# Optimization experiments

Measured on AMD Instinct MI355X. Metric: run time of the kernel, lower is better.

The kernel has to match this reference:

```python
import jax, jax.numpy as jnp
import numpy as np

DIM = 96
HEADS = 6
HEAD_DIM = DIM // HEADS
WIN = 8
N = WIN * WIN           # tokens per window
B_ = 4096               # num_windows * batch
TABLE = (2 * WIN - 1) ** 2  # 225


def setup_inputs() -> dict:
    key = jax.random.key(0)
    ks = jax.random.split(key, 7)
    x = jax.random.normal(ks[0], (B_, N, DIM), dtype=jnp.float32)
    rpi = jax.random.randint(ks[1], (N, N), 0, TABLE)
    qkv_w = jax.random.normal(ks[2], (3 * DIM, DIM), dtype=jnp.float32) * 0.02
    qkv_b = jnp.zeros((3 * DIM,), dtype=jnp.float32)
    proj_w = jax.random.normal(ks[3], (DIM, DIM), dtype=jnp.float32) * 0.02
    proj_b = jnp.zeros((DIM,), dtype=jnp.float32)
    rpb_table = jax.random.normal(ks[4], (TABLE, HEADS), dtype=jnp.float32) * 0.02
    return {"x": x, "rpi": rpi, "qkv_w": qkv_w, "qkv_b": qkv_b,
            "proj_w": proj_w, "proj_b": proj_b, "rpb_table": rpb_table}


def reference(x, rpi, qkv_w, qkv_b, proj_w, proj_b, rpb_table):
    b_, n, c = x.shape
    scale = HEAD_DIM ** -0.5
    # qkv projection: (b_, n, 3, H, hd)
    qkv = (x @ qkv_w.T + qkv_b).reshape(b_, n, 3, HEADS, HEAD_DIM)
    qkv = jnp.transpose(qkv, (2, 0, 3, 1, 4))  # (3, b_, H, n, hd)
    q, k, v = qkv[0], qkv[1], qkv[2]
    attn = jnp.einsum('bhnd,bhmd->bhnm', q * scale, k)
    # relative position bias gather: (n, n, H) -> (H, n, n)
    bias = jnp.transpose(rpb_table[rpi], (2, 0, 1))
    attn = jax.nn.softmax(attn + bias[None], axis=-1)
    out = jnp.einsum('bhnm,bhmd->bnhd', attn, v).reshape(b_, n, c)
    return out @ proj_w.T + proj_b
```

## Files before the change

### kernel.cpp

```cpp
#include <hip/hip_runtime.h>

#define NWIN 4096
#define DIM 96
#define HEADS 6
#define NTOK 64

typedef __bf16 bf16x8 __attribute__((ext_vector_type(8)));
typedef __bf16 bf16x4 __attribute__((ext_vector_type(4)));
typedef short  s16x4  __attribute__((ext_vector_type(4)));
typedef float  f32x4  __attribute__((ext_vector_type(4)));

#define WS_QKVW 0
#define WS_PROJW 55296
#define WS_BIAS 73728
#define WS_TOTAL 172032

__device__ __forceinline__ f32x4 mfma32(bf16x8 a, bf16x8 b, f32x4 c) {
  return __builtin_amdgcn_mfma_f32_16x16x32_bf16(a, b, c, 0, 0, 0);
}
__device__ __forceinline__ f32x4 mfma16k(bf16x4 a, bf16x4 b, f32x4 c) {
  return __builtin_amdgcn_mfma_f32_16x16x16bf16_1k(
      __builtin_bit_cast(s16x4, a), __builtin_bit_cast(s16x4, b), c, 0, 0, 0);
}

__device__ __forceinline__ bf16x8 cvt8(const float* p) {
  const float4* q = (const float4*)p;
  float4 a = q[0];
  float4 b = q[1];
  bf16x8 r;
  r[0] = (__bf16)a.x; r[1] = (__bf16)a.y; r[2] = (__bf16)a.z; r[3] = (__bf16)a.w;
  r[4] = (__bf16)b.x; r[5] = (__bf16)b.y; r[6] = (__bf16)b.z; r[7] = (__bf16)b.w;
  return r;
}

__global__ void prep_kernel(const float* __restrict__ qkv_w,
                            const float* __restrict__ proj_w,
                            const float* __restrict__ rpb,
                            const int* __restrict__ rpi,
                            char* __restrict__ ws) {
  int i = blockIdx.x * blockDim.x + threadIdx.x;
  __bf16* qw = (__bf16*)(ws + WS_QKVW);
  __bf16* pw = (__bf16*)(ws + WS_PROJW);
  float* bias = (float*)(ws + WS_BIAS);
  if (i < 288 * 96) qw[i] = (__bf16)qkv_w[i];
  int j = i - 288 * 96;
  if (j >= 0 && j < 96 * 96) pw[j] = (__bf16)proj_w[j];
  int t = i - (288 * 96 + 96 * 96);
  if (t >= 0 && t < HEADS * 16 * 64 * 4) {
    int r = t & 3;
    int lane = (t >> 2) & 63;
    int ba = (t >> 8) & 15;
    int h = t >> 12;
    int bq = ba >> 2, a = ba & 3;
    int l16 = lane & 15, lq = lane >> 4;
    int qrow = 16 * bq + l16;
    int kcol = 16 * a + 4 * lq + r;
    bias[t] = rpb[rpi[qrow * 64 + kcol] * HEADS + h];
  }
}

template <bool USE_WS>
__global__ __launch_bounds__(384, 4) void win_attn(
    const float* __restrict__ x,
    const int* __restrict__ rpi,
    const float* __restrict__ qkv_w,
    const float* __restrict__ qkv_b,
    const float* __restrict__ proj_w,
    const float* __restrict__ proj_b,
    const float* __restrict__ rpb,
    const char* __restrict__ ws,
    float* __restrict__ out) {
  __shared__ __align__(16) __bf16 lds[6656 + HEADS * 1152];

  const int tid = (int)threadIdx.x;
  const int wv = tid >> 6;
  const int lane = tid & 63;
  const int l16 = lane & 15;
  const int lq = lane >> 4;
  const int b = (int)blockIdx.x;

  __bf16* xfrag = lds;
  __bf16* ao = lds;
  __bf16* vh = lds + 6656 + wv * 1152;
  __bf16* Pt = vh;

  const float* xw = x + (size_t)b * (NTOK * DIM);
  const __bf16* qwb = (const __bf16*)(ws + WS_QKVW);
  const __bf16* pwb = (const __bf16*)(ws + WS_PROJW);
  const float4* bias4 = (const float4*)(ws + WS_BIAS) + (wv << 10);

#pragma unroll
  for (int ff = 0; ff < 2; ++ff) {
    const int f = 2 * wv + ff;
    const int mt = f / 3, ks = f - 3 * mt;
    bf16x8 v = cvt8(xw + (16 * mt + l16) * DIM + 32 * ks + 8 * lq);
    *(bf16x8*)(xfrag + (f * 64 + lane) * 8) = v;
  }
  __syncthreads();

#define XV(mt, ks) (*(const bf16x8*)(xfrag + (((mt) * 3 + (ks)) * 64 + lane) * 8))

  bf16x4 kb[4];
  {
    const int frow = (HEADS + wv) * 16;
    bf16x8 wb[3];
#pragma unroll
    for (int ks = 0; ks < 3; ++ks) {
      if constexpr (USE_WS)
        wb[ks] = *(const bf16x8*)(qwb + (frow + l16) * 96 + 32 * ks + 8 * lq);
      else
        wb[ks] = cvt8(qkv_w + (frow + l16) * 96 + 32 * ks + 8 * lq);
    }
    const float4 kb4 = *(const float4*)(qkv_b + frow + 4 * lq);
    const float kbv[4] = {kb4.x, kb4.y, kb4.z, kb4.w};
#pragma unroll
    for (int mt = 0; mt < 4; ++mt) {
      f32x4 acc = {0.f, 0.f, 0.f, 0.f};
#pragma unroll
      for (int ks = 0; ks < 3; ++ks) acc = mfma32(wb[ks], XV(mt, ks), acc);
#pragma unroll
      for (int r = 0; r < 4; ++r) kb[mt][r] = (__bf16)(acc[r] + kbv[r]);
    }
  }

  bf16x4 qv4[4];
  {
    const int frow = wv * 16;
    bf16x8 wb[3];
#pragma unroll
    for (int ks = 0; ks < 3; ++ks) {
      if constexpr (USE_WS)
        wb[ks] = *(const bf16x8*)(qwb + (frow + l16) * 96 + 32 * ks + 8 * lq);
      else
        wb[ks] = cvt8(qkv_w + (frow + l16) * 96 + 32 * ks + 8 * lq);
    }
    const float4 qb4 = *(const float4*)(qkv_b + frow + 4 * lq);
    const float qbv[4] = {qb4.x, qb4.y, qb4.z, qb4.w};
#pragma unroll
    for (int mt = 0; mt < 4; ++mt) {
      f32x4 acc = {0.f, 0.f, 0.f, 0.f};
#pragma unroll
      for (int ks = 0; ks < 3; ++ks) acc = mfma32(wb[ks], XV(mt, ks), acc);
#pragma unroll
      for (int r = 0; r < 4; ++r) qv4[mt][r] = (__bf16)((acc[r] + qbv[r]) * 0.25f);
    }
  }

  {
    const int frow = (2 * HEADS + wv) * 16;
    bf16x8 wb[3];
#pragma unroll
    for (int ks = 0; ks < 3; ++ks) {
      if constexpr (USE_WS)
        wb[ks] = *(const bf16x8*)(qwb + (frow + l16) * 96 + 32 * ks + 8 * lq);
      else
        wb[ks] = cvt8(qkv_w + (frow + l16) * 96 + 32 * ks + 8 * lq);
    }
    const float vb = qkv_b[frow + l16];
#pragma unroll
    for (int mt = 0; mt < 4; ++mt) {
      f32x4 acc = {0.f, 0.f, 0.f, 0.f};
#pragma unroll
      for (int ks = 0; ks < 3; ++ks) acc = mfma32(XV(mt, ks), wb[ks], acc);
      bf16x4 t;
#pragma unroll
      for (int r = 0; r < 4; ++r) t[r] = (__bf16)(acc[r] + vb);
      *(bf16x4*)(vh + l16 * 72 + 16 * mt + 4 * lq) = t;
    }
  }
  asm volatile("s_waitcnt lgkmcnt(0)" ::: "memory");
  bf16x8 vbf[2];
#pragma unroll
  for (int c = 0; c < 2; ++c)
    vbf[c] = *(const bf16x8*)(vh + l16 * 72 + 32 * c + 8 * lq);

  __syncthreads();

  f32x4 bn[4];
  if constexpr (USE_WS) {
#pragma unroll
    for (int a = 0; a < 4; ++a) {
      float4 t = bias4[a * 64 + lane];
      bn[a][0] = t.x; bn[a][1] = t.y; bn[a][2] = t.z; bn[a][3] = t.w;
    }
  }

#pragma unroll
  for (int bq = 0; bq < 4; ++bq) {
    f32x4 s[4];
    if constexpr (USE_WS) {
#pragma unroll
      for (int a = 0; a < 4; ++a) s[a] = bn[a];
      if (bq < 3) {
#pragma unroll
        for (int a = 0; a < 4; ++a) {
          float4 t = bias4[((bq + 1) * 4 + a) * 64 + lane];
          bn[a][0] = t.x; bn[a][1] = t.y; bn[a][2] = t.z; bn[a][3] = t.w;
        }
      }
    } else {
#pragma unroll
      for (int a = 0; a < 4; ++a)
#pragma unroll
        for (int r = 0; r < 4; ++r)
          s[a][r] = rpb[rpi[(16 * bq + l16) * 64 + 16 * a + 4 * lq + r] * HEADS + wv];
    }

#pragma unroll
    for (int a = 0; a < 4; ++a) s[a] = mfma16k(kb[a], qv4[bq], s[a]);

    float tp[4];
#pragma unroll
    for (int a = 0; a < 4; ++a) {
      float t0 = 0.f;
#pragma unroll
      for (int r = 0; r < 4; ++r) {
        float e = __expf(s[a][r]);
        s[a][r] = e;
        t0 += e;
      }
      tp[a] = t0;
    }
    float tsum = (tp[0] + tp[1]) + (tp[2] + tp[3]);
    tsum += __shfl_xor(tsum, 16);
    tsum += __shfl_xor(tsum, 32);
    const float rv = 1.0f / tsum;

#pragma unroll
    for (int a = 0; a < 4; ++a) {
      bf16x4 p;
#pragma unroll
      for (int r = 0; r < 4; ++r) p[r] = (__bf16)(s[a][r] * rv);
      *(bf16x4*)(Pt + (2 * a + (lq >> 1)) * 128 + l16 * 8 + (lq & 1) * 4) = p;
    }
    asm volatile("s_waitcnt lgkmcnt(0)" ::: "memory");

    f32x4 oacc = {0.f, 0.f, 0.f, 0.f};
#pragma unroll
    for (int c = 0; c < 2; ++c) {
      const bf16x8 pa = *(const bf16x8*)(Pt + c * 512 + lane * 8);
      oacc = mfma32(pa, vbf[c], oacc);
    }
    asm volatile("s_waitcnt lgkmcnt(0)" ::: "memory");

#pragma unroll
    for (int r = 0; r < 4; ++r)
      ao[(16 * bq + 4 * lq + r) * 104 + 16 * wv + l16] = (__bf16)oacc[r];
  }
  __syncthreads();

  bf16x8 wpb[3];
#pragma unroll
  for (int ks = 0; ks < 3; ++ks) {
    if constexpr (USE_WS)
      wpb[ks] = *(const bf16x8*)(pwb + (16 * wv + l16) * 96 + 32 * ks + 8 * lq);
    else
      wpb[ks] = cvt8(proj_w + (16 * wv + l16) * 96 + 32 * ks + 8 * lq);
  }
  const float pb2 = proj_b[16 * wv + l16];
  float* outw = out + (size_t)b * (NTOK * DIM);
#pragma unroll
  for (int mt = 0; mt < 4; ++mt) {
    f32x4 acc = {0.f, 0.f, 0.f, 0.f};
#pragma unroll
    for (int ks = 0; ks < 3; ++ks) {
      bf16x8 aa = *(const bf16x8*)(ao + (16 * mt + l16) * 104 + 32 * ks + 8 * lq);
      acc = mfma32(aa, wpb[ks], acc);
    }
#pragma unroll
    for (int r = 0; r < 4; ++r)
      outw[(16 * mt + 4 * lq + r) * 96 + 16 * wv + l16] = acc[r] + pb2;
  }
}

extern "C" void kernel_launch(void* const* d_in, const int* in_sizes, int n_in,
                              void* d_out, int out_size, void* d_ws, size_t ws_size,
                              hipStream_t stream) {
  const float* x      = (const float*)d_in[0];
  const int*   rpi    = (const int*)d_in[1];
  const float* qkv_w  = (const float*)d_in[2];
  const float* qkv_b  = (const float*)d_in[3];
  const float* proj_w = (const float*)d_in[4];
  const float* proj_b = (const float*)d_in[5];
  const float* rpb    = (const float*)d_in[6];
  float* out = (float*)d_out;

  if (ws_size >= (size_t)WS_TOTAL) {
    prep_kernel<<<240, 256, 0, stream>>>(qkv_w, proj_w, rpb, rpi, (char*)d_ws);
    win_attn<true><<<NWIN, 384, 0, stream>>>(x, rpi, qkv_w, qkv_b, proj_w,
                                             proj_b, rpb, (const char*)d_ws, out);
  } else {
    win_attn<false><<<NWIN, 384, 0, stream>>>(x, rpi, qkv_w, qkv_b, proj_w,
                                              proj_b, rpb, (const char*)d_ws, out);
  }
}
```

Baseline: 82.01 us.

## Keep V and softmax probabilities in registers, feed PV MFMA directly

```diff
diff --git a/kernel.cpp b/kernel.cpp
--- a/kernel.cpp
+++ b/kernel.cpp
@@ -70,7 +70,7 @@
     const float* __restrict__ rpb,
     const char* __restrict__ ws,
     float* __restrict__ out) {
-  __shared__ __align__(16) __bf16 lds[6656 + HEADS * 1152];
+  __shared__ __align__(16) __bf16 lds[6656];
 
   const int tid = (int)threadIdx.x;
   const int wv = tid >> 6;
@@ -81,8 +81,6 @@
 
   __bf16* xfrag = lds;
   __bf16* ao = lds;
-  __bf16* vh = lds + 6656 + wv * 1152;
-  __bf16* Pt = vh;
 
   const float* xw = x + (size_t)b * (NTOK * DIM);
   const __bf16* qwb = (const __bf16*)(ws + WS_QKVW);
@@ -146,6 +144,7 @@
     }
   }
 
+  bf16x4 vb4[4];
   {
     const int frow = (2 * HEADS + wv) * 16;
     bf16x8 wb[3];
@@ -162,18 +161,11 @@
       f32x4 acc = {0.f, 0.f, 0.f, 0.f};
 #pragma unroll
       for (int ks = 0; ks < 3; ++ks) acc = mfma32(XV(mt, ks), wb[ks], acc);
-      bf16x4 t;
-#pragma unroll
-      for (int r = 0; r < 4; ++r) t[r] = (__bf16)(acc[r] + vb);
-      *(bf16x4*)(vh + l16 * 72 + 16 * mt + 4 * lq) = t;
-    }
-  }
-  asm volatile("s_waitcnt lgkmcnt(0)" ::: "memory");
-  bf16x8 vbf[2];
-#pragma unroll
-  for (int c = 0; c < 2; ++c)
-    vbf[c] = *(const bf16x8*)(vh + l16 * 72 + 32 * c + 8 * lq);
-
+#pragma unroll
+      for (int r = 0; r < 4; ++r) vb4[mt][r] = (__bf16)(acc[r] + vb);
+    }
+  }
+#undef XV
   __syncthreads();
 
   f32x4 bn[4];
@@ -210,13 +202,14 @@
     for (int a = 0; a < 4; ++a) s[a] = mfma16k(kb[a], qv4[bq], s[a]);
 
     float tp[4];
+    bf16x4 pa[4];
 #pragma unroll
     for (int a = 0; a < 4; ++a) {
       float t0 = 0.f;
 #pragma unroll
       for (int r = 0; r < 4; ++r) {
         float e = __expf(s[a][r]);
-        s[a][r] = e;
+        pa[a][r] = (__bf16)e;
         t0 += e;
       }
       tp[a] = t0;
@@ -224,28 +217,15 @@
     float tsum = (tp[0] + tp[1]) + (tp[2] + tp[3]);
     tsum += __shfl_xor(tsum, 16);
     tsum += __shfl_xor(tsum, 32);
+
+    f32x4 oacc = {0.f, 0.f, 0.f, 0.f};
+#pragma unroll
+    for (int a = 0; a < 4; ++a) oacc = mfma16k(pa[a], vb4[a], oacc);
+
     const float rv = 1.0f / tsum;
-
-#pragma unroll
-    for (int a = 0; a < 4; ++a) {
-      bf16x4 p;
-#pragma unroll
-      for (int r = 0; r < 4; ++r) p[r] = (__bf16)(s[a][r] * rv);
-      *(bf16x4*)(Pt + (2 * a + (lq >> 1)) * 128 + l16 * 8 + (lq & 1) * 4) = p;
-    }
-    asm volatile("s_waitcnt lgkmcnt(0)" ::: "memory");
-
-    f32x4 oacc = {0.f, 0.f, 0.f, 0.f};
-#pragma unroll
-    for (int c = 0; c < 2; ++c) {
-      const bf16x8 pa = *(const bf16x8*)(Pt + c * 512 + lane * 8);
-      oacc = mfma32(pa, vbf[c], oacc);
-    }
-    asm volatile("s_waitcnt lgkmcnt(0)" ::: "memory");
-
 #pragma unroll
     for (int r = 0; r < 4; ++r)
-      ao[(16 * bq + 4 * lq + r) * 104 + 16 * wv + l16] = (__bf16)oacc[r];
+      ao[(16 * bq + 4 * lq + r) * 104 + 16 * wv + l16] = (__bf16)(oacc[r] * rv);
   }
   __syncthreads();
 
```

New measurement: 82.67 us. No clear change (+0.8%).
